# Kernel tuning notes

Measured on AMD Instinct MI355X. Metric: run time of the kernel, lower is better.

The kernel has to match this reference:

```python
import jax, jax.numpy as jnp
import numpy as np

EPS = 1e-12  # matches torch F.normalize eps


def _l2_normalize(x):
    # F.normalize(x, p=2, dim=1): divide by clamped norm
    norm = jnp.sqrt(jnp.sum(x * x, axis=1, keepdims=True))
    return x / jnp.maximum(norm, EPS)


def setup_inputs() -> dict:
    key = jax.random.key(0)
    k1, k2, k3 = jax.random.split(key, 3)
    N, D, P, C = 16384, 768, 2048, 1000
    h = jax.random.normal(k1, (N, D), dtype=jnp.float32)
    prototypes = jax.random.normal(k2, (P, D), dtype=jnp.float32) * 0.1
    prototype_class = jax.random.normal(k3, (P, C), dtype=jnp.float32)
    temperature = jnp.float32(1.0)
    return {"h": h, "prototypes": prototypes,
            "prototype_class": prototype_class, "temperature": temperature}


def reference(h, prototypes, prototype_class, temperature):
    h_norm = _l2_normalize(h)                      # [N, D]
    p_norm = _l2_normalize(prototypes)             # [P, D]
    # cdist (p=2): sqrt(||a||^2 + ||b||^2 - 2 a.b), clamped at 0
    h_sq = jnp.sum(h_norm * h_norm, axis=1, keepdims=True)   # [N, 1]
    p_sq = jnp.sum(p_norm * p_norm, axis=1)                  # [P]
    dots = jnp.einsum('nd,pd->np', h_norm, p_norm)           # [N, P]
    dist_sq = jnp.maximum(h_sq + p_sq[None, :] - 2.0 * dots, 0.0)
    distances = jnp.sqrt(dist_sq)                            # [N, P]
    tau = jax.nn.softplus(temperature)
    activations = jnp.exp(-tau * distances)                  # [N, P]
    class_logits = jnp.matmul(activations, prototype_class)  # [N, C]
    return class_logits
```

## Files before the change

kernel.cpp:

```cpp
#include <hip/hip_runtime.h>
#include <hip/hip_bf16.h>
#include <math.h>

typedef unsigned short ushort_t;
typedef unsigned char uchar_t;
typedef unsigned int uint_t;
typedef __attribute__((ext_vector_type(8))) short bf16x8;
typedef __attribute__((ext_vector_type(4))) float f32x4;

#define AS1 __attribute__((address_space(1)))
#define AS3 __attribute__((address_space(3)))

__device__ __forceinline__ void gld_lds16(const void* g, void* l) {
  __builtin_amdgcn_global_load_lds((const AS1 void*)g, (AS3 void*)l, 16, 0, 0);
}

__device__ __forceinline__ ushort_t f32_to_bf16_bits(float v) {
  __hip_bfloat16 b = __float2bfloat16(v);
  return *(ushort_t*)&b;
}

__device__ __forceinline__ uint_t pack_fp8x4(float4 v, float sc) {
  int r = __builtin_amdgcn_cvt_pk_fp8_f32(v.x * sc, v.y * sc, 0, false);
  r = __builtin_amdgcn_cvt_pk_fp8_f32(v.z * sc, v.w * sc, r, true);
  return (uint_t)r;
}


__global__ __launch_bounds__(256) void prep(const float4* __restrict__ h,
                                            uchar_t* __restrict__ h8, int rowsH,
                                            const float4* __restrict__ p,
                                            uchar_t* __restrict__ p8, int rowsP,
                                            const float* __restrict__ pc,
                                            ushort_t* __restrict__ pcT,
                                            int P, int C, int normBlocks) {
  __shared__ float tile[32][33];
  if ((int)blockIdx.x < normBlocks) {
    int r = (blockIdx.x * 256 + threadIdx.x) >> 6;
    const int lane = threadIdx.x & 63;
    const float4* xr;
    uchar_t* o8;
    if (r < rowsH) {
      xr = h + (size_t)r * 192;
      o8 = h8;
    } else {
      r -= rowsH;
      if (r >= rowsP) return;
      xr = p + (size_t)r * 192;
      o8 = p8;
    }
    float4 v0 = xr[lane];
    float4 v1 = xr[lane + 64];
    float4 v2 = xr[lane + 128];
    float ss = v0.x * v0.x + v0.y * v0.y + v0.z * v0.z + v0.w * v0.w
             + v1.x * v1.x + v1.y * v1.y + v1.z * v1.z + v1.w * v1.w
             + v2.x * v2.x + v2.y * v2.y + v2.z * v2.z + v2.w * v2.w;
#pragma unroll
    for (int off = 32; off > 0; off >>= 1) ss += __shfl_xor(ss, off, 64);
    const float sc = 4.0f / fmaxf(sqrtf(ss), 1e-12f);
    const int rb = r >> 4, rl = r & 15;
    const int key = (rl >> 1) & 7;
    const int cc = (lane & 15) >> 1;
    const int cphys = ((cc ^ key) << 3) + ((lane & 1) << 2);
    const int ktb = lane >> 4;
    uchar_t* rowbase = o8 + (size_t)rb * 12 * 1024 + rl * 64 + cphys;
    *(uint_t*)(rowbase + (size_t)(ktb) * 1024)     = pack_fp8x4(v0, sc);
    *(uint_t*)(rowbase + (size_t)(4 + ktb) * 1024) = pack_fp8x4(v1, sc);
    *(uint_t*)(rowbase + (size_t)(8 + ktb) * 1024) = pack_fp8x4(v2, sc);
  } else {
    const int b = blockIdx.x - normBlocks;
    const int nkb = P / 32;
    const int bk = b % nkb, bc = b / nkb;
    const int k0 = bk * 32, c0 = bc * 32;
    const int tx = threadIdx.x & 31, ty = threadIdx.x >> 5;
#pragma unroll
    for (int rr = 0; rr < 4; ++rr) {
      const int c = c0 + tx;
      tile[ty + rr * 8][tx] = (c < C) ? pc[(size_t)(k0 + ty + rr * 8) * C + c] : 0.f;
    }
    __syncthreads();
    const int c2 = tx >> 3, off = tx & 7;
#pragma unroll
    for (int rr = 0; rr < 4; ++rr) {
      const int row = c0 + ty + rr * 8;
      const int rb = row >> 4, rl = row & 15;
      const int key4 = (rl >> 1) & 3;
      size_t us = (((size_t)rb * nkb + bk) * 16 + rl) * 32 + ((c2 ^ key4) << 3) + off;
      pcT[us] = f32_to_bf16_bits(tile[tx][ty + rr * 8]);
    }
  }
}

__launch_bounds__(256)
__global__ void gemm1_fp8(const uchar_t* __restrict__ A, const uchar_t* __restrict__ B,
                          ushort_t* __restrict__ act, const float* __restrict__ tptr,
                          int nKt, int actKT, int gx, int gxlog2) {
  __shared__ __align__(16) uchar_t As[16384];
  __shared__ __align__(16) uchar_t Bs[16384];
  const int tid = threadIdx.x, lane = tid & 63, wave = tid >> 6;
  const int wm = wave >> 1, wn = wave & 1;
  const int lid = blockIdx.x, xcd = lid & 7, q = lid >> 3;
  const int t = q & (gx - 1);
  const int s = ((q >> gxlog2) << 3) | xcd;

  f32x4 acc[4][4];
#pragma unroll
  for (int i = 0; i < 4; ++i)
#pragma unroll
    for (int j = 0; j < 4; ++j) acc[i][j] = (f32x4){0.f, 0.f, 0.f, 0.f};

  const uchar_t* aW = A + ((size_t)(s * 8 + 2 * wave) * nKt) * 1024 + lane * 16;
  const uchar_t* bW = B + ((size_t)(t * 8 + 2 * wave) * nKt) * 1024 + lane * 16;
  const size_t rstride = (size_t)nKt * 1024;
  uchar_t* lA = &As[wave * 4096];
  uchar_t* lB = &Bs[wave * 4096];

  const int fr = lane & 15, g = lane >> 4;
  const int key = (fr >> 1) & 7;
  const int rowoff = fr * 64;
  const int cp0 = ((g ^ key) << 3);
  const int cp1 = (((g | 4) ^ key) << 3);

  const int nIter = nKt >> 1;
  for (int kt = 0; kt < nIter; ++kt) {
    const size_t koff = (size_t)(2 * kt) * 1024;
    __syncthreads();
    gld_lds16(aW + koff, lA);
    gld_lds16(aW + koff + 1024, lA + 1024);
    gld_lds16(aW + rstride + koff, lA + 2048);
    gld_lds16(aW + rstride + koff + 1024, lA + 3072);
    gld_lds16(bW + koff, lB);
    gld_lds16(bW + koff + 1024, lB + 1024);
    gld_lds16(bW + rstride + koff, lB + 2048);
    gld_lds16(bW + rstride + koff + 1024, lB + 3072);
    __syncthreads();

#pragma unroll
    for (int kk = 0; kk < 2; ++kk) {
#pragma unroll
      for (int ksub = 0; ksub < 2; ++ksub) {
        const int cp = ksub ? cp1 : cp0;
        long a[4], b[4];
#pragma unroll
        for (int i = 0; i < 4; ++i)
          a[i] = *(const long*)&As[((wm * 4 + i) * 2 + kk) * 1024 + rowoff + cp];
#pragma unroll
        for (int j = 0; j < 4; ++j)
          b[j] = *(const long*)&Bs[((wn * 4 + j) * 2 + kk) * 1024 + rowoff + cp];
#pragma unroll
        for (int i = 0; i < 4; ++i)
#pragma unroll
          for (int j = 0; j < 4; ++j)
            acc[i][j] = __builtin_amdgcn_mfma_f32_16x16x32_fp8_fp8(a[i], b[j], acc[i][j], 0, 0, 0);
      }
    }
  }

  float tmp = *tptr;
  const float tau = log1pf(expf(tmp));
  const int crow = g * 4, ccol = fr;
  const int rowB = s * 128 + wm * 64, colB = t * 128 + wn * 64;
#pragma unroll
  for (int i = 0; i < 4; ++i)
#pragma unroll
    for (int j = 0; j < 4; ++j) {
      const int col = colB + j * 16 + ccol;
      const size_t ktile = col >> 5;
      const int c2 = (col >> 3) & 3, co = col & 7;
#pragma unroll
      for (int rr = 0; rr < 4; ++rr) {
        const int row = rowB + i * 16 + crow + rr;
        const int rb = row >> 4, rl = row & 15;
        const int key4 = (rl >> 1) & 3;
        float d2 = fmaxf(2.0f - acc[i][j][rr] * 0.125f, 0.0f);
        float a = __expf(-tau * sqrtf(d2));
        act[(((size_t)rb * actKT + ktile) * 16 + rl) * 32 + ((c2 ^ key4) << 3) + co] =
            f32_to_bf16_bits(a);
      }
    }
}

__launch_bounds__(256)
__global__ void gemm2_bf16(const ushort_t* __restrict__ A, const ushort_t* __restrict__ B,
                           float* __restrict__ out, int nKt, int ldc, int ncols,
                           int gx, int gxlog2) {
  __shared__ __align__(16) ushort_t As[8192];
  __shared__ __align__(16) ushort_t Bs[8192];
  const int tid = threadIdx.x, lane = tid & 63, wave = tid >> 6;
  const int wm = wave >> 1, wn = wave & 1;
  const int lid = blockIdx.x, xcd = lid & 7, q = lid >> 3;
  const int t = q & (gx - 1);
  const int s = ((q >> gxlog2) << 3) | xcd;

  f32x4 acc[4][4];
#pragma unroll
  for (int i = 0; i < 4; ++i)
#pragma unroll
    for (int j = 0; j < 4; ++j) acc[i][j] = (f32x4){0.f, 0.f, 0.f, 0.f};

  const ushort_t* aW = A + ((size_t)(s * 8 + 2 * wave) * nKt) * 512 + lane * 8;
  const ushort_t* bW = B + ((size_t)(t * 8 + 2 * wave) * nKt) * 512 + lane * 8;
  const size_t rstride = (size_t)nKt * 512;
  ushort_t* lA = &As[wave * 2048];
  ushort_t* lB = &Bs[wave * 2048];

  const int fr = lane & 15, g = lane >> 4;
  const int key4 = (fr >> 1) & 3;
  const int cph = (g ^ key4) << 3;
  const int rowoff = fr * 32;

  const int nIter = nKt >> 1;
  for (int kt = 0; kt < nIter; ++kt) {
    const size_t koff = (size_t)(2 * kt) * 512;
    __syncthreads();
    gld_lds16(aW + koff, lA);
    gld_lds16(aW + koff + 512, lA + 512);
    gld_lds16(aW + rstride + koff, lA + 1024);
    gld_lds16(aW + rstride + koff + 512, lA + 1536);
    gld_lds16(bW + koff, lB);
    gld_lds16(bW + koff + 512, lB + 512);
    gld_lds16(bW + rstride + koff, lB + 1024);
    gld_lds16(bW + rstride + koff + 512, lB + 1536);
    __syncthreads();

#pragma unroll
    for (int kk = 0; kk < 2; ++kk) {
      bf16x8 af[4], bfr[4];
#pragma unroll
      for (int i = 0; i < 4; ++i)
        af[i] = *(const bf16x8*)&As[((wm * 4 + i) * 2 + kk) * 512 + rowoff + cph];
#pragma unroll
      for (int j = 0; j < 4; ++j)
        bfr[j] = *(const bf16x8*)&Bs[((wn * 4 + j) * 2 + kk) * 512 + rowoff + cph];
#pragma unroll
      for (int i = 0; i < 4; ++i)
#pragma unroll
        for (int j = 0; j < 4; ++j)
          acc[i][j] = __builtin_amdgcn_mfma_f32_16x16x32_bf16(af[i], bfr[j], acc[i][j], 0, 0, 0);
    }
  }

  const int crow = g * 4, ccol = fr;
  const int rowB = s * 128 + wm * 64, colB = t * 128 + wn * 64;
#pragma unroll
  for (int i = 0; i < 4; ++i)
#pragma unroll
    for (int j = 0; j < 4; ++j) {
      const int col = colB + j * 16 + ccol;
      if (col < ncols) {
#pragma unroll
        for (int rr = 0; rr < 4; ++rr) {
          const int row = rowB + i * 16 + crow + rr;
          out[(size_t)row * ldc + col] = acc[i][j][rr];
        }
      }
    }
}

extern "C" void kernel_launch(void* const* d_in, const int* in_sizes, int n_in,
                              void* d_out, int out_size, void* d_ws, size_t ws_size,
                              hipStream_t stream) {
  const float* h    = (const float*)d_in[0];
  const float* prot = (const float*)d_in[1];
  const float* pc   = (const float*)d_in[2];
  const float* temp = (const float*)d_in[3];
  float* out = (float*)d_out;

  const int D = 768;
  const int N = in_sizes[0] / D;
  const int P = in_sizes[1] / D;
  const int C = in_sizes[2] / P;
  const int CP = (C + 127) & ~127;

  char* ws = (char*)d_ws;
  size_t off = 0;
  uchar_t* h8   = (uchar_t*)(ws + off); off += (size_t)N * D;
  uchar_t* p8   = (uchar_t*)(ws + off); off += (size_t)P * D;
  ushort_t* pcT = (ushort_t*)(ws + off); off += (size_t)CP * P * 2;
  ushort_t* act = (ushort_t*)(ws + off); off += (size_t)N * P * 2;
  (void)ws_size;

  const int normBlocks = (N + P) / 4;
  const int transBlocks = (P / 32) * (CP / 32);
  prep<<<normBlocks + transBlocks, 256, 0, stream>>>(
      (const float4*)h, h8, N, (const float4*)prot, p8, P,
      pc, pcT, P, C, normBlocks);

  {
    const int GX = P / 128, GY = N / 128;
    gemm1_fp8<<<GX * GY, 256, 0, stream>>>(h8, p8, act, temp, D / 64, P / 32, GX, 4);
  }
  {
    const int GX = CP / 128, GY = N / 128;
    gemm2_bf16<<<GX * GY, 256, 0, stream>>>(act, pcT, out, P / 32, C, C, GX, 3);
  }
}
```

Before: 244.9 us.

## Rewrite second GEMM as 256x256 double-buffered 8-wave phased pipeline

Replaces the 128x128, 4-wave, single-buffered bf16 GEMM with a 256x256-tile, 8-wave kernel. It double-buffers K tiles of 64 in 128KB of LDS and splits each K step into four phases that interleave global-to-LDS prefetch, LDS reads and MFMA bursts, using explicit barriers, vmcnt waits and s_setprio. The larger tile raises operand reuse and the phasing aims to hide load latency behind compute. The costs are fewer blocks (64x4 grid), heavy LDS use that limits occupancy, and hardcoded layout shifts that assume P=2048 and CP=1024.

```diff
diff --git a/kernel.cpp b/kernel.cpp
--- a/kernel.cpp
+++ b/kernel.cpp
@@ -180,79 +180,116 @@
     }
 }
 
-__launch_bounds__(256)
-__global__ void gemm2_bf16(const ushort_t* __restrict__ A, const ushort_t* __restrict__ B,
-                           float* __restrict__ out, int nKt, int ldc, int ncols,
-                           int gx, int gxlog2) {
-  __shared__ __align__(16) ushort_t As[8192];
-  __shared__ __align__(16) ushort_t Bs[8192];
+#define BARRIER() do { asm volatile("" ::: "memory"); __builtin_amdgcn_s_barrier(); \
+                       asm volatile("" ::: "memory"); } while (0)
+#define LGKM0()   asm volatile("s_waitcnt lgkmcnt(0)" ::: "memory")
+#define VM6()     asm volatile("s_waitcnt vmcnt(6)" ::: "memory")
+#define VM0()     asm volatile("s_waitcnt vmcnt(0)" ::: "memory")
+#define PRIO1()   __builtin_amdgcn_s_setprio(1)
+#define PRIO0()   __builtin_amdgcn_s_setprio(0)
+#define MM(a, b, c) __builtin_amdgcn_mfma_f32_16x16x32_bf16(a, b, c, 0, 0, 0)
+
+#define PHASE_MFMA(I0, I1, A00, A01, A10, A11)                                   \
+  acc[I0][0] = MM(A00, b00, acc[I0][0]); acc[I0][1] = MM(A00, b10, acc[I0][1]);  \
+  acc[I0][2] = MM(A00, b20, acc[I0][2]); acc[I0][3] = MM(A00, b30, acc[I0][3]);  \
+  acc[I1][0] = MM(A10, b00, acc[I1][0]); acc[I1][1] = MM(A10, b10, acc[I1][1]);  \
+  acc[I1][2] = MM(A10, b20, acc[I1][2]); acc[I1][3] = MM(A10, b30, acc[I1][3]);  \
+  acc[I0][0] = MM(A01, b01, acc[I0][0]); acc[I0][1] = MM(A01, b11, acc[I0][1]);  \
+  acc[I0][2] = MM(A01, b21, acc[I0][2]); acc[I0][3] = MM(A01, b31, acc[I0][3]);  \
+  acc[I1][0] = MM(A11, b01, acc[I1][0]); acc[I1][1] = MM(A11, b11, acc[I1][1]);  \
+  acc[I1][2] = MM(A11, b21, acc[I1][2]); acc[I1][3] = MM(A11, b31, acc[I1][3])
+
+__launch_bounds__(512, 2)
+__global__ void gemm2_bf16_8ph(const ushort_t* __restrict__ A,
+                               const ushort_t* __restrict__ B,
+                               float* __restrict__ out, int ldc, int ncols,
+                               int nKt) {
+  __shared__ __align__(16) uchar_t sm[131072];
   const int tid = threadIdx.x, lane = tid & 63, wave = tid >> 6;
-  const int wm = wave >> 1, wn = wave & 1;
+  const int wm = wave >> 2, wn = wave & 3;
   const int lid = blockIdx.x, xcd = lid & 7, q = lid >> 3;
-  const int t = q & (gx - 1);
-  const int s = ((q >> gxlog2) << 3) | xcd;
-
-  f32x4 acc[4][4];
-#pragma unroll
-  for (int i = 0; i < 4; ++i)
+  const int tb = q & 3, sb = ((q >> 2) << 3) | xcd;
+
+  f32x4 acc[8][4];
+#pragma unroll
+  for (int i = 0; i < 8; ++i)
 #pragma unroll
     for (int j = 0; j < 4; ++j) acc[i][j] = (f32x4){0.f, 0.f, 0.f, 0.f};
 
-  const ushort_t* aW = A + ((size_t)(s * 8 + 2 * wave) * nKt) * 512 + lane * 8;
-  const ushort_t* bW = B + ((size_t)(t * 8 + 2 * wave) * nKt) * 512 + lane * 8;
-  const size_t rstride = (size_t)nKt * 512;
-  ushort_t* lA = &As[wave * 2048];
-  ushort_t* lB = &Bs[wave * 2048];
+  const int lw = wave & 1, rw = wave >> 1;
+  const uchar_t* Apl = (const uchar_t*)A + ((size_t)(sb * 16) << 16) + (lw << 10) + lane * 16;
+  const uchar_t* Bpl = (const uchar_t*)B + ((size_t)(tb * 16) << 16) + (lw << 10) + lane * 16;
 
   const int fr = lane & 15, g = lane >> 4;
-  const int key4 = (fr >> 1) & 3;
-  const int cph = (g ^ key4) << 3;
-  const int rowoff = fr * 32;
-
-  const int nIter = nKt >> 1;
-  for (int kt = 0; kt < nIter; ++kt) {
-    const size_t koff = (size_t)(2 * kt) * 512;
-    __syncthreads();
-    gld_lds16(aW + koff, lA);
-    gld_lds16(aW + koff + 512, lA + 512);
-    gld_lds16(aW + rstride + koff, lA + 1024);
-    gld_lds16(aW + rstride + koff + 512, lA + 1536);
-    gld_lds16(bW + koff, lB);
-    gld_lds16(bW + koff + 512, lB + 512);
-    gld_lds16(bW + rstride + koff, lB + 1024);
-    gld_lds16(bW + rstride + koff + 512, lB + 1536);
-    __syncthreads();
-
-#pragma unroll
-    for (int kk = 0; kk < 2; ++kk) {
-      bf16x8 af[4], bfr[4];
-#pragma unroll
-      for (int i = 0; i < 4; ++i)
-        af[i] = *(const bf16x8*)&As[((wm * 4 + i) * 2 + kk) * 512 + rowoff + cph];
-#pragma unroll
-      for (int j = 0; j < 4; ++j)
-        bfr[j] = *(const bf16x8*)&Bs[((wn * 4 + j) * 2 + kk) * 512 + rowoff + cph];
-#pragma unroll
-      for (int i = 0; i < 4; ++i)
-#pragma unroll
-        for (int j = 0; j < 4; ++j)
-          acc[i][j] = __builtin_amdgcn_mfma_f32_16x16x32_bf16(af[i], bfr[j], acc[i][j], 0, 0, 0);
-    }
-  }
-
-  const int crow = g * 4, ccol = fr;
-  const int rowB = s * 128 + wm * 64, colB = t * 128 + wn * 64;
-#pragma unroll
-  for (int i = 0; i < 4; ++i)
+  const int rdoff = fr * 64 + ((g ^ ((fr >> 1) & 3)) << 4);
+  const int wm8 = wm * 8, wn4 = wn * 4;
+
+#define STA(r_, T_, bo_) gld_lds16(Apl + (((size_t)(r_) << 16) + ((size_t)(T_) << 11)), \
+                                   sm + (bo_) + ((((r_) << 1) + lw) << 10))
+#define STB(r_, T_, bo_) gld_lds16(Bpl + (((size_t)(r_) << 16) + ((size_t)(T_) << 11)), \
+                                   sm + (bo_) + 32768 + ((((r_) << 1) + lw) << 10))
+#define DSA(i_, l_) (*(const bf16x8*)(sm + bufoff + (((wm8 + (i_)) * 2 + (l_)) << 10) + rdoff))
+#define DSB(j_, l_) (*(const bf16x8*)(sm + bufoff + 32768 + (((wn4 + (j_)) * 2 + (l_)) << 10) + rdoff))
+
+  STB(rw, 0, 0); STB(rw + 4, 0, 0); STB(rw + 8, 0, 0); STB(rw + 12, 0, 0);
+  STA(rw, 0, 0); STA(rw + 8, 0, 0); STA(rw + 4, 0, 0); STA(rw + 12, 0, 0);
+  STB(rw, 1, 65536); STB(rw + 4, 1, 65536); STB(rw + 8, 1, 65536); STB(rw + 12, 1, 65536);
+  STA(rw, 1, 65536); STA(rw + 8, 1, 65536);
+  VM6(); BARRIER();
+
+  for (int kt = 0; kt < nKt; ++kt) {
+    const int bufoff = (kt & 1) << 16;
+    const int nbo = ((kt + 1) & 1) << 16;
+    bf16x8 b00 = DSB(0, 0), b01 = DSB(0, 1), b10 = DSB(1, 0), b11 = DSB(1, 1);
+    bf16x8 b20 = DSB(2, 0), b21 = DSB(2, 1), b30 = DSB(3, 0), b31 = DSB(3, 1);
+    bf16x8 a00 = DSA(0, 0), a01 = DSA(0, 1), a10 = DSA(1, 0), a11 = DSA(1, 1);
+    if (kt + 1 < nKt) { STA(rw + 4, kt + 1, nbo); STA(rw + 12, kt + 1, nbo); }
+    BARRIER(); LGKM0();
+    PRIO1();
+    PHASE_MFMA(0, 1, a00, a01, a10, a11);
+    PRIO0();
+    BARRIER();
+    {
+      bf16x8 a20 = DSA(2, 0), a21 = DSA(2, 1), a30 = DSA(3, 0), a31 = DSA(3, 1);
+      if (kt + 2 < nKt) { STB(rw, kt + 2, bufoff); STB(rw + 4, kt + 2, bufoff); }
+      BARRIER(); LGKM0();
+      PRIO1();
+      PHASE_MFMA(2, 3, a20, a21, a30, a31);
+      PRIO0();
+      BARRIER();
+    }
+    {
+      bf16x8 a40 = DSA(4, 0), a41 = DSA(4, 1), a50 = DSA(5, 0), a51 = DSA(5, 1);
+      if (kt + 2 < nKt) { STB(rw + 8, kt + 2, bufoff); STB(rw + 12, kt + 2, bufoff); }
+      BARRIER(); LGKM0();
+      PRIO1();
+      PHASE_MFMA(4, 5, a40, a41, a50, a51);
+      PRIO0();
+      BARRIER();
+    }
+    {
+      bf16x8 a60 = DSA(6, 0), a61 = DSA(6, 1), a70 = DSA(7, 0), a71 = DSA(7, 1);
+      if (kt + 2 < nKt) { STA(rw, kt + 2, bufoff); STA(rw + 8, kt + 2, bufoff); }
+      BARRIER(); LGKM0();
+      PRIO1();
+      PHASE_MFMA(6, 7, a60, a61, a70, a71);
+      PRIO0();
+      if (kt + 2 < nKt) { VM6(); } else { VM0(); }
+      BARRIER();
+    }
+  }
+
+  const int crow = g * 4;
+  const int rowB = sb * 256 + wm * 128, colB = tb * 256 + wn * 64;
+#pragma unroll
+  for (int i = 0; i < 8; ++i)
 #pragma unroll
     for (int j = 0; j < 4; ++j) {
-      const int col = colB + j * 16 + ccol;
+      const int col = colB + j * 16 + fr;
       if (col < ncols) {
 #pragma unroll
-        for (int rr = 0; rr < 4; ++rr) {
-          const int row = rowB + i * 16 + crow + rr;
-          out[(size_t)row * ldc + col] = acc[i][j][rr];
-        }
+        for (int rr = 0; rr < 4; ++rr)
+          out[(size_t)(rowB + i * 16 + crow + rr) * ldc + col] = acc[i][j][rr];
       }
     }
 }
@@ -291,7 +328,7 @@
     gemm1_fp8<<<GX * GY, 256, 0, stream>>>(h8, p8, act, temp, D / 64, P / 32, GX, 4);
   }
   {
-    const int GX = CP / 128, GY = N / 128;
-    gemm2_bf16<<<GX * GY, 256, 0, stream>>>(act, pcT, out, P / 32, C, C, GX, 3);
-  }
-}
+    const int GX = CP / 256, GY = N / 256;
+    gemm2_bf16_8ph<<<GX * GY, 512, 0, stream>>>(act, pcT, out, C, C, P / 64);
+  }
+}
```

After: 230.8 us. -5.8%, faster.
